# Kernel optimization log

Measured on AMD Instinct MI355X. Metric: run time of the kernel, lower is better.

## Reference

```python
import jax, jax.numpy as jnp
import numpy as np

B, L, H, V = 32, 2048, 128, 32000
ALPHA = 0.95
GATE_THRESH = 0.7
LN_EPS = 1e-5
NORM_EPS = 1e-12


def setup_inputs() -> dict:
    key = jax.random.key(0)
    ks = jax.random.split(key, 12)
    s = 0.02
    return {
        "seq": jax.random.randint(ks[0], (B, L), 0, V),
        "embed_w": jax.random.normal(ks[1], (V, H), jnp.float32) * s,
        "ff_w1": jax.random.normal(ks[2], (2 * H, H), jnp.float32) * s,
        "ff_b1": jnp.zeros((2 * H,), jnp.float32),
        "ff_w2": jax.random.normal(ks[3], (H, 2 * H), jnp.float32) * s,
        "ff_b2": jnp.zeros((H,), jnp.float32),
        "ln_g": jnp.ones((H,), jnp.float32),
        "ln_b": jnp.zeros((H,), jnp.float32),
        "kp_w": jax.random.normal(ks[4], (H, H), jnp.float32) * s,
        "rp_w": jax.random.normal(ks[5], (H, H), jnp.float32) * s,
        "rp_b": jnp.zeros((H,), jnp.float32),
        "out_w": jax.random.normal(ks[6], (V, H), jnp.float32) * s,
        "out_b": jnp.zeros((V,), jnp.float32),
    }


def reference(seq, embed_w, ff_w1, ff_b1, ff_w2, ff_b2, ln_g, ln_b,
              kp_w, rp_w, rp_b, out_w, out_b):
    h = embed_w[seq]                                    # (B,L,H)
    ff = jnp.maximum(h @ ff_w1.T + ff_b1, 0.0) @ ff_w2.T + ff_b2
    x = h + ff
    mu = jnp.mean(x, axis=-1, keepdims=True)
    var = jnp.mean((x - mu) ** 2, axis=-1, keepdims=True)
    h = (x - mu) * jax.lax.rsqrt(var + LN_EPS) * ln_g + ln_b

    k_all = jnp.einsum('blh,oh->blo', h, kp_w)          # kp(h), (B,L,H)
    ks_seq = jnp.transpose(k_all[:, :-1, :], (1, 0, 2)) # (L-1,B,H)

    def step(M, k):
        kn = k / jnp.maximum(jnp.linalg.norm(k, axis=-1, keepdims=True), NORM_EPS)
        vp = jnp.einsum('bij,bj->bi', M, kn)
        err = k - vp
        fire = (jnp.linalg.norm(err, axis=-1)
                >= GATE_THRESH * jnp.linalg.norm(k, axis=-1)).astype(k.dtype)
        delta = fire[:, None, None] * err[:, :, None] * kn[:, None, :]
        return M + (1.0 - ALPHA) * delta, None

    M0 = jnp.zeros((B, H, H), h.dtype)
    M, _ = jax.lax.scan(step, M0, ks_seq)

    q = k_all[:, -1, :]                                 # (B,H)
    read = jnp.einsum('bij,bj->bi', M, q)
    r = read @ rp_w.T + rp_b
    return r @ out_w.T + out_b                          # (B,V)
```

## Files before the change

kernel.cpp:

```cpp
#include <hip/hip_runtime.h>
#include <hip/hip_fp16.h>

#define B_  32
#define L_  2048
#define H_  128
#define H2_ 256
#define V_  32000
#define NT_ (B_*L_)
#define TOKS_PER_BLK 64
#define W_  32
#define NW_ (L_/W_)

template<int CTRL, int RMASK>
__device__ __forceinline__ float dpp_add(float x) {
    int v = __builtin_amdgcn_update_dpp(0, __float_as_int(x), CTRL, RMASK, 0xf, true);
    return x + __int_as_float(v);
}
__device__ __forceinline__ float wave_sum63(float x) {
    x = dpp_add<0x111, 0xf>(x);
    x = dpp_add<0x112, 0xf>(x);
    x = dpp_add<0x114, 0xf>(x);
    x = dpp_add<0x118, 0xf>(x);
    x = dpp_add<0x142, 0xa>(x);
    x = dpp_add<0x143, 0xc>(x);
    return x;
}
__device__ __forceinline__ float wave_allsum(float x) {
    x = wave_sum63(x);
    return __int_as_float(__builtin_amdgcn_readlane(__float_as_int(x), 63));
}
__device__ __forceinline__ float quad_sum(float x) {
    int v = __builtin_amdgcn_update_dpp(0, __float_as_int(x), 0xB1, 0xf, 0xf, true);
    x += __int_as_float(v);
    v = __builtin_amdgcn_update_dpp(0, __float_as_int(x), 0x4E, 0xf, 0xf, true);
    return x + __int_as_float(v);
}
__device__ __forceinline__ float sum16_hi(float x) {
    x = dpp_add<0x111, 0xf>(x);
    x = dpp_add<0x112, 0xf>(x);
    x = dpp_add<0x114, 0xf>(x);
    x = dpp_add<0x118, 0xf>(x);
    return x;
}

__global__ __launch_bounds__(256, 2) void ka_ff_ln_kp(
    const int*   __restrict__ seq,   const float* __restrict__ embed_w,
    const float* __restrict__ ff_w1, const float* __restrict__ ff_b1,
    const float* __restrict__ ff_w2, const float* __restrict__ ff_b2,
    const float* __restrict__ ln_g,  const float* __restrict__ ln_b,
    const float* __restrict__ kp_w,  float* __restrict__ k_all)
{
    __shared__ __half2 w1p[64][256];
    __shared__ float2 h2[128];
    __shared__ float2 y12[256];
    __shared__ float  p_sh[2][2][128];
    __shared__ float2 hln2[128];
    __shared__ float  red_sh[8];

    const int tid  = threadIdx.x;
    const int half = tid >> 7;
    const int i    = tid & 127;
    const int lane = tid & 63;
    const int wave = tid >> 6;

    for (int idx = tid; idx < 64*256; idx += 256) {
        int o = idx >> 6, j2 = idx & 63;
        float2 ab = *(const float2*)(ff_w1 + o*128 + 2*j2);
        w1p[j2][o] = __floats2half2_rn(ab.x, ab.y);
    }
    __half2 w2r[64];
    {
        const float* src = ff_w2 + (size_t)i*H2_ + half*128;
        #pragma unroll
        for (int q4 = 0; q4 < 16; ++q4) {
            float4 a = *(const float4*)(src + q4*8);
            float4 b = *(const float4*)(src + q4*8 + 4);
            w2r[q4*4+0] = __floats2half2_rn(a.x, a.y);
            w2r[q4*4+1] = __floats2half2_rn(a.z, a.w);
            w2r[q4*4+2] = __floats2half2_rn(b.x, b.y);
            w2r[q4*4+3] = __floats2half2_rn(b.z, b.w);
        }
    }
    float kreg[64];
    {
        const float* src = kp_w + (size_t)i*H_ + half*64;
        #pragma unroll
        for (int j4 = 0; j4 < 16; ++j4) {
            float4 v = *(const float4*)(src + j4*4);
            kreg[j4*4+0]=v.x; kreg[j4*4+1]=v.y; kreg[j4*4+2]=v.z; kreg[j4*4+3]=v.w;
        }
    }
    const float b1v = ff_b1[tid];
    const float b2v = ff_b2[i];
    const float gv  = ln_g[i];
    const float bv  = ln_b[i];
    __syncthreads();

    const int base = blockIdx.x * TOKS_PER_BLK;
    for (int it = 0; it < TOKS_PER_BLK; it += 2) {
        const int t0 = base + it;
        if (tid < 64) {
            int tok = tid >> 5;
            int l32 = tid & 31;
            int v   = seq[t0 + tok];
            float4 hv = *(const float4*)(embed_w + (size_t)v*H_ + l32*4);
            ((float*)&h2[l32*4+0])[tok] = hv.x;
            ((float*)&h2[l32*4+1])[tok] = hv.y;
            ((float*)&h2[l32*4+2])[tok] = hv.z;
            ((float*)&h2[l32*4+3])[tok] = hv.w;
        }
        __syncthreads();
        float a0 = b1v, a1 = b1v;
        #pragma unroll
        for (int j2 = 0; j2 < 64; ++j2) {
            __half2 w = w1p[j2][tid];
            float4 hh = *(const float4*)&h2[2*j2];
            float wl = __low2float(w), wh = __high2float(w);
            a0 = fmaf(wl, hh.x, a0); a0 = fmaf(wh, hh.z, a0);
            a1 = fmaf(wl, hh.y, a1); a1 = fmaf(wh, hh.w, a1);
        }
        y12[tid] = make_float2(fmaxf(a0, 0.f), fmaxf(a1, 0.f));
        __syncthreads();
        float c0 = 0.f, c1 = 0.f;
        #pragma unroll
        for (int q = 0; q < 64; ++q) {
            __half2 w = w2r[q];
            float4 yy = *(const float4*)&y12[half*128 + 2*q];
            float wl = __low2float(w), wh = __high2float(w);
            c0 = fmaf(wl, yy.x, c0); c0 = fmaf(wh, yy.z, c0);
            c1 = fmaf(wl, yy.y, c1); c1 = fmaf(wh, yy.w, c1);
        }
        p_sh[half][0][i] = c0;
        p_sh[half][1][i] = c1;
        __syncthreads();
        float x = ((const float*)&h2[i])[half] + p_sh[0][half][i] + p_sh[1][half][i] + b2v;
        {
            float s = x, s2 = x*x;
            #pragma unroll
            for (int m = 1; m <= 32; m <<= 1) {
                s  += __shfl_xor(s,  m);
                s2 += __shfl_xor(s2, m);
            }
            if (lane == 0) { red_sh[wave*2] = s; red_sh[wave*2+1] = s2; }
        }
        __syncthreads();
        float mu  = (red_sh[half*4+0] + red_sh[half*4+2]) * (1.0f/128.0f);
        float ex2 = (red_sh[half*4+1] + red_sh[half*4+3]) * (1.0f/128.0f);
        float var = ex2 - mu*mu;
        float rstd = 1.0f / sqrtf(var + 1e-5f);
        float hln = (x - mu) * rstd * gv + bv;
        ((float*)&hln2[i])[half] = hln;
        __syncthreads();
        float k0 = 0.f, k1 = 0.f;
        #pragma unroll
        for (int jj = 0; jj < 64; ++jj) {
            float2 hh = hln2[half*64 + jj];
            k0 = fmaf(kreg[jj], hh.x, k0);
            k1 = fmaf(kreg[jj], hh.y, k1);
        }
        p_sh[half][0][i] = k0;
        p_sh[half][1][i] = k1;
        __syncthreads();
        if (tid < 128) {
            k_all[(size_t)t0*H_     + i] = p_sh[0][0][i] + p_sh[1][0][i];
            k_all[(size_t)(t0+1)*H_ + i] = p_sh[0][1][i] + p_sh[1][1][i];
        }
    }
}

__global__ __launch_bounds__(512, 2) void kc_scan(
    const float* __restrict__ k_all, const float* __restrict__ rp_w,
    const float* __restrict__ rp_b,  float* __restrict__ r_out)
{
    __shared__ __align__(16) float kch[2][W_*H_];
    __shared__ __align__(16) float P_lds[W_][H_];
    __shared__ __align__(16) float G_T[W_][34];
    __shared__ __align__(16) float escT[H_][34];
    __shared__ __align__(16) float read_sh[H_];
    __shared__ float pr_sh[2][H_];

    const int b    = blockIdx.x;
    const int tid  = threadIdx.x;
    const int lane = tid & 63;
    const int wv   = tid >> 6;
    const int r    = tid >> 2;
    const int s    = tid & 3;
    const int cb   = s << 5;
    const int gi   = tid >> 4;
    const int gc   = (tid & 15) << 3;

    const float* kb = k_all + (size_t)b * (L_*H_);

    float Mreg[32];
    #pragma unroll
    for (int m = 0; m < 32; ++m) Mreg[m] = 0.f;

    {
        float4 a = *(const float4*)(kb + tid*8);
        float4 c = *(const float4*)(kb + tid*8 + 4);
        *(float4*)&kch[0][tid*8]     = a;
        *(float4*)&kch[0][tid*8 + 4] = c;
    }
    __syncthreads();

    #pragma unroll 1
    for (int w = 0; w < NW_; ++w) {
        const int buf = w & 1;
        const float* kcur = kch[buf];
        const float* kprv = kch[buf^1];

        float4 st0, st1;
        if (w + 1 < NW_) {
            const float* src = kb + (size_t)(w+1)*(W_*H_) + tid*8;
            st0 = *(const float4*)(src);
            st1 = *(const float4*)(src + 4);
        }

        if (w > 0) {
            #pragma unroll
            for (int j2 = 0; j2 < 16; ++j2) {
                float2 e2 = *(const float2*)&escT[r][2*j2];
                const float* ka0 = kprv + (2*j2)*H_ + cb;
                const float* ka1 = kprv + (2*j2+1)*H_ + cb;
                #pragma unroll
                for (int m8 = 0; m8 < 8; ++m8) {
                    const int a = ((m8 + 2*s) & 7) << 2;
                    float4 kv0 = *(const float4*)(ka0 + a);
                    float4 kv1 = *(const float4*)(ka1 + a);
                    Mreg[m8*4+0] = fmaf(e2.x, kv0.x, Mreg[m8*4+0]);
                    Mreg[m8*4+1] = fmaf(e2.x, kv0.y, Mreg[m8*4+1]);
                    Mreg[m8*4+2] = fmaf(e2.x, kv0.z, Mreg[m8*4+2]);
                    Mreg[m8*4+3] = fmaf(e2.x, kv0.w, Mreg[m8*4+3]);
                    Mreg[m8*4+0] = fmaf(e2.y, kv1.x, Mreg[m8*4+0]);
                    Mreg[m8*4+1] = fmaf(e2.y, kv1.y, Mreg[m8*4+1]);
                    Mreg[m8*4+2] = fmaf(e2.y, kv1.z, Mreg[m8*4+2]);
                    Mreg[m8*4+3] = fmaf(e2.y, kv1.w, Mreg[m8*4+3]);
                }
            }
        }
        __syncthreads();

        if (w + 1 < NW_) {
            *(float4*)&kch[buf^1][tid*8]     = st0;
            *(float4*)&kch[buf^1][tid*8 + 4] = st1;
        }

        {
            float4 kia = *(const float4*)(kcur + gi*H_ + gc);
            float4 kib = *(const float4*)(kcur + gi*H_ + gc + 4);
            #pragma unroll
            for (int j = 0; j < W_; ++j) {
                const float* kj = kcur + j*H_;
                float p0=0.f, p1=0.f, p2=0.f, p3=0.f;
                #pragma unroll
                for (int m8 = 0; m8 < 8; ++m8) {
                    const int a = ((m8 + 2*s) & 7) << 2;
                    float4 kv = *(const float4*)(kj + cb + a);
                    p0 = fmaf(Mreg[m8*4+0], kv.x, p0);
                    p1 = fmaf(Mreg[m8*4+1], kv.y, p1);
                    p2 = fmaf(Mreg[m8*4+2], kv.z, p2);
                    p3 = fmaf(Mreg[m8*4+3], kv.w, p3);
                }
                float p = quad_sum((p0+p1) + (p2+p3));
                if (s == 0) P_lds[j][r] = p;
                float4 ga = *(const float4*)(kj + gc);
                float4 gb = *(const float4*)(kj + gc + 4);
                float g0 = kia.x*ga.x + kia.y*ga.y;
                g0 = fmaf(kia.z, ga.z, g0); g0 = fmaf(kia.w, ga.w, g0);
                float g1 = kib.x*gb.x + kib.y*gb.y;
                g1 = fmaf(kib.z, gb.z, g1); g1 = fmaf(kib.w, gb.w, g1);
                float g = sum16_hi(g0 + g1);
                if ((tid & 15) == 15) G_T[j][gi] = g;
            }
        }
        __syncthreads();

        if (wv == 0) {
            const int last = (w == NW_-1);
            #pragma unroll
            for (int j = 0; j < W_; ++j) {
                float nk2 = G_T[j][j];
                float rn  = 1.0f / fmaxf(sqrtf(nk2), 1e-12f);
                float t0 = P_lds[j][lane];
                float t1 = P_lds[j][lane + 64];
                float k0 = kcur[j*H_ + lane];
                float k1 = kcur[j*H_ + 64 + lane];
                #pragma unroll
                for (int i2 = 0; i2 < ((j+1)>>1); ++i2) {
                    float2 g2 = *(const float2*)&G_T[j][2*i2];
                    float2 ea = *(const float2*)&escT[lane][2*i2];
                    float2 eb = *(const float2*)&escT[lane+64][2*i2];
                    t0 = fmaf(g2.x, ea.x, t0); t1 = fmaf(g2.x, eb.x, t1);
                    if (2*i2+1 < j) {
                        t0 = fmaf(g2.y, ea.y, t0); t1 = fmaf(g2.y, eb.y, t1);
                    }
                }
                if (last && j == W_-1) {
                    read_sh[lane]      = t0;
                    read_sh[lane + 64] = t1;
                } else {
                    float e0 = fmaf(-rn, t0, k0);
                    float e1 = fmaf(-rn, t1, k1);
                    float es = wave_allsum(fmaf(e0, e0, e1*e1));
                    float sc = (es >= 0.49f * nk2) ? 0.05f * rn : 0.f;
                    escT[lane][j]      = sc * e0;
                    escT[lane + 64][j] = sc * e1;
                }
            }
        }
        __syncthreads();
    }

    if (tid < 256) {
        const int o  = tid & 127;
        const int hf = tid >> 7;
        float acc = 0.f;
        #pragma unroll
        for (int j4 = 0; j4 < 16; ++j4) {
            float4 wvv = *(const float4*)(rp_w + (size_t)o*H_ + hf*64 + j4*4);
            float4 rv  = *(const float4*)&read_sh[hf*64 + j4*4];
            acc = fmaf(wvv.x, rv.x, acc);
            acc = fmaf(wvv.y, rv.y, acc);
            acc = fmaf(wvv.z, rv.z, acc);
            acc = fmaf(wvv.w, rv.w, acc);
        }
        pr_sh[hf][o] = acc;
    }
    __syncthreads();
    if (tid < 128) r_out[b*H_ + tid] = pr_sh[0][tid] + pr_sh[1][tid] + rp_b[tid];
}

__global__ __launch_bounds__(256) void kd_out(
    const float* __restrict__ r_in, const float* __restrict__ out_w,
    const float* __restrict__ out_b, float* __restrict__ out)
{
    __shared__ float r_sh[B_ * H_];
    const int tid = threadIdx.x;
    for (int idx = tid; idx < B_*H_; idx += 256) r_sh[idx] = r_in[idx];
    __syncthreads();
    const int v = blockIdx.x * 256 + tid;
    const float* wrow = out_w + (size_t)v * H_;
    float acc[B_];
    #pragma unroll
    for (int bb = 0; bb < B_; ++bb) acc[bb] = 0.f;
    for (int h4 = 0; h4 < H_/4; ++h4) {
        float4 w = *(const float4*)(wrow + h4*4);
        #pragma unroll
        for (int bb = 0; bb < B_; ++bb) {
            const float* rr = &r_sh[bb*H_ + h4*4];
            acc[bb] = fmaf(w.x, rr[0], acc[bb]);
            acc[bb] = fmaf(w.y, rr[1], acc[bb]);
            acc[bb] = fmaf(w.z, rr[2], acc[bb]);
            acc[bb] = fmaf(w.w, rr[3], acc[bb]);
        }
    }
    const float bias = out_b[v];
    #pragma unroll
    for (int bb = 0; bb < B_; ++bb) out[(size_t)bb*V_ + v] = acc[bb] + bias;
}

extern "C" void kernel_launch(void* const* d_in, const int* in_sizes, int n_in,
                              void* d_out, int out_size, void* d_ws, size_t ws_size,
                              hipStream_t stream)
{
    const int*   seq     = (const int*)  d_in[0];
    const float* embed_w = (const float*)d_in[1];
    const float* ff_w1   = (const float*)d_in[2];
    const float* ff_b1   = (const float*)d_in[3];
    const float* ff_w2   = (const float*)d_in[4];
    const float* ff_b2   = (const float*)d_in[5];
    const float* ln_g    = (const float*)d_in[6];
    const float* ln_b    = (const float*)d_in[7];
    const float* kp_w    = (const float*)d_in[8];
    const float* rp_w    = (const float*)d_in[9];
    const float* rp_b    = (const float*)d_in[10];
    const float* out_w   = (const float*)d_in[11];
    const float* out_b   = (const float*)d_in[12];
    float* out = (float*)d_out;

    float* k_all = (float*)d_ws;
    float* r_buf = k_all + (size_t)NT_ * H_;

    ka_ff_ln_kp<<<dim3(NT_/TOKS_PER_BLK), dim3(256), 0, stream>>>(
        seq, embed_w, ff_w1, ff_b1, ff_w2, ff_b2, ln_g, ln_b, kp_w, k_all);
    kc_scan<<<dim3(B_), dim3(512), 0, stream>>>(k_all, rp_w, rp_b, r_buf);
    kd_out<<<dim3(V_/256), dim3(256), 0, stream>>>(r_buf, out_w, out_b, out);
}
```

Before: 1.932 ms.

## Restructure scan kernel to 1024 threads with overlapped Gram computation

The scan kernel now runs with 1024 threads, and each thread holds a 2x8 tile of M instead of a 32-wide row slice. This removes the quad reduction in favour of 16-lane reductions. The Gram matrix for the next window is computed by waves 1-8 while wave 0 runs the serial error recurrence, so it leaves the critical path. Wave 0 keeps the error vectors in registers and reads Gram entries through readlane rather than LDS. The k chunks use padded rows to avoid LDS bank conflicts. In exchange the kernel raises register pressure in wave 0 and adds work at its wider launch.

Result: faster. 1.637 ms (-15.3%).

```diff
diff --git a/kernel.cpp b/kernel.cpp
--- a/kernel.cpp
+++ b/kernel.cpp
@@ -10,6 +10,7 @@
 #define TOKS_PER_BLK 64
 #define W_  32
 #define NW_ (L_/W_)
+#define KROW 132
 
 template<int CTRL, int RMASK>
 __device__ __forceinline__ float dpp_add(float x) {
@@ -28,12 +29,6 @@
 __device__ __forceinline__ float wave_allsum(float x) {
     x = wave_sum63(x);
     return __int_as_float(__builtin_amdgcn_readlane(__float_as_int(x), 63));
-}
-__device__ __forceinline__ float quad_sum(float x) {
-    int v = __builtin_amdgcn_update_dpp(0, __float_as_int(x), 0xB1, 0xf, 0xf, true);
-    x += __int_as_float(v);
-    v = __builtin_amdgcn_update_dpp(0, __float_as_int(x), 0x4E, 0xf, 0xf, true);
-    return x + __int_as_float(v);
 }
 __device__ __forceinline__ float sum16_hi(float x) {
     x = dpp_add<0x111, 0xf>(x);
@@ -168,145 +163,169 @@
     }
 }
 
-__global__ __launch_bounds__(512, 2) void kc_scan(
+__global__ __launch_bounds__(1024, 4) void kc_scan(
     const float* __restrict__ k_all, const float* __restrict__ rp_w,
     const float* __restrict__ rp_b,  float* __restrict__ r_out)
 {
-    __shared__ __align__(16) float kch[2][W_*H_];
+    __shared__ __align__(16) float kch[2][W_*KROW];
     __shared__ __align__(16) float P_lds[W_][H_];
-    __shared__ __align__(16) float G_T[W_][34];
-    __shared__ __align__(16) float escT[H_][34];
+    __shared__ __align__(16) float escT[W_][H_];
+    __shared__ __align__(16) float G_lds[2][64][16];
     __shared__ __align__(16) float read_sh[H_];
     __shared__ float pr_sh[2][H_];
 
-    const int b    = blockIdx.x;
     const int tid  = threadIdx.x;
     const int lane = tid & 63;
     const int wv   = tid >> 6;
-    const int r    = tid >> 2;
-    const int s    = tid & 3;
-    const int cb   = s << 5;
-    const int gi   = tid >> 4;
-    const int gc   = (tid & 15) << 3;
-
-    const float* kb = k_all + (size_t)b * (L_*H_);
-
-    float Mreg[32];
+    const int ct   = tid & 15;
+    const int rt   = tid >> 4;
+    const int cb   = ct << 3;
+    const int srow = tid >> 5;
+    const int scol = (tid & 31) << 2;
+
+    const float* kb = k_all + (size_t)blockIdx.x * (L_*H_);
+
+    float M0[8], M1[8];
     #pragma unroll
-    for (int m = 0; m < 32; ++m) Mreg[m] = 0.f;
+    for (int c = 0; c < 8; ++c) { M0[c] = 0.f; M1[c] = 0.f; }
 
     {
-        float4 a = *(const float4*)(kb + tid*8);
-        float4 c = *(const float4*)(kb + tid*8 + 4);
-        *(float4*)&kch[0][tid*8]     = a;
-        *(float4*)&kch[0][tid*8 + 4] = c;
+        float4 v = *(const float4*)(kb + tid*4);
+        *(float4*)&kch[0][srow*KROW + scol] = v;
+    }
+    __syncthreads();
+
+    if (wv >= 1 && wv <= 8) {
+        const int p0i = (wv-1)*128 + lane*2;
+        const int gi  = p0i >> 5;
+        const int gj0 = p0i & 31;
+        const float* ki  = &kch[0][gi*KROW];
+        const float* kj0 = &kch[0][gj0*KROW];
+        const float* kj1 = &kch[0][(gj0+1)*KROW];
+        float d00=0,d01=0,d02=0,d03=0, d10=0,d11=0,d12=0,d13=0;
+        #pragma unroll 8
+        for (int c4 = 0; c4 < 32; ++c4) {
+            float4 x = *(const float4*)(ki  + c4*4);
+            float4 y = *(const float4*)(kj0 + c4*4);
+            float4 z = *(const float4*)(kj1 + c4*4);
+            d00=fmaf(x.x,y.x,d00); d01=fmaf(x.y,y.y,d01);
+            d02=fmaf(x.z,y.z,d02); d03=fmaf(x.w,y.w,d03);
+            d10=fmaf(x.x,z.x,d10); d11=fmaf(x.y,z.y,d11);
+            d12=fmaf(x.z,z.z,d12); d13=fmaf(x.w,z.w,d13);
+        }
+        G_lds[0][gi     ][gj0>>1] = (d00+d01)+(d02+d03);
+        G_lds[0][gi + 32][gj0>>1] = (d10+d11)+(d12+d13);
     }
     __syncthreads();
 
     #pragma unroll 1
     for (int w = 0; w < NW_; ++w) {
         const int buf = w & 1;
-        const float* kcur = kch[buf];
-        const float* kprv = kch[buf^1];
-
-        float4 st0, st1;
-        if (w + 1 < NW_) {
-            const float* src = kb + (size_t)(w+1)*(W_*H_) + tid*8;
-            st0 = *(const float4*)(src);
-            st1 = *(const float4*)(src + 4);
-        }
+        const float* kcur = &kch[buf][0];
+        const float* kprv = &kch[buf^1][0];
+        const bool hn = (w + 1 < NW_);
+        float4 stg;
+        if (hn) stg = *(const float4*)(kb + (size_t)(w+1)*(W_*H_) + tid*4);
 
         if (w > 0) {
+            #pragma unroll 8
+            for (int j = 0; j < W_; ++j) {
+                float2 e2 = *(const float2*)&escT[j][2*rt];
+                const float* kr = kprv + j*KROW + cb;
+                float4 a  = *(const float4*)(kr);
+                float4 b2 = *(const float4*)(kr + 4);
+                M0[0]=fmaf(e2.x,a.x,M0[0]);  M0[1]=fmaf(e2.x,a.y,M0[1]);
+                M0[2]=fmaf(e2.x,a.z,M0[2]);  M0[3]=fmaf(e2.x,a.w,M0[3]);
+                M0[4]=fmaf(e2.x,b2.x,M0[4]); M0[5]=fmaf(e2.x,b2.y,M0[5]);
+                M0[6]=fmaf(e2.x,b2.z,M0[6]); M0[7]=fmaf(e2.x,b2.w,M0[7]);
+                M1[0]=fmaf(e2.y,a.x,M1[0]);  M1[1]=fmaf(e2.y,a.y,M1[1]);
+                M1[2]=fmaf(e2.y,a.z,M1[2]);  M1[3]=fmaf(e2.y,a.w,M1[3]);
+                M1[4]=fmaf(e2.y,b2.x,M1[4]); M1[5]=fmaf(e2.y,b2.y,M1[5]);
+                M1[6]=fmaf(e2.y,b2.z,M1[6]); M1[7]=fmaf(e2.y,b2.w,M1[7]);
+            }
+        }
+        __syncthreads();
+        if (hn) *(float4*)&kch[buf^1][srow*KROW + scol] = stg;
+
+        #pragma unroll 8
+        for (int j = 0; j < W_; ++j) {
+            const float* kr = kcur + j*KROW + cb;
+            float4 a  = *(const float4*)(kr);
+            float4 b2 = *(const float4*)(kr + 4);
+            float p0 = M0[0]*a.x;
+            p0=fmaf(M0[1],a.y,p0);  p0=fmaf(M0[2],a.z,p0);  p0=fmaf(M0[3],a.w,p0);
+            p0=fmaf(M0[4],b2.x,p0); p0=fmaf(M0[5],b2.y,p0);
+            p0=fmaf(M0[6],b2.z,p0); p0=fmaf(M0[7],b2.w,p0);
+            float p1 = M1[0]*a.x;
+            p1=fmaf(M1[1],a.y,p1);  p1=fmaf(M1[2],a.z,p1);  p1=fmaf(M1[3],a.w,p1);
+            p1=fmaf(M1[4],b2.x,p1); p1=fmaf(M1[5],b2.y,p1);
+            p1=fmaf(M1[6],b2.z,p1); p1=fmaf(M1[7],b2.w,p1);
+            p0 = sum16_hi(p0);
+            p1 = sum16_hi(p1);
+            if (ct == 15) *(float2*)&P_lds[j][2*rt] = make_float2(p0, p1);
+        }
+        __syncthreads();
+
+        if (wv == 0) {
+            float Grf[16];
             #pragma unroll
-            for (int j2 = 0; j2 < 16; ++j2) {
-                float2 e2 = *(const float2*)&escT[r][2*j2];
-                const float* ka0 = kprv + (2*j2)*H_ + cb;
-                const float* ka1 = kprv + (2*j2+1)*H_ + cb;
-                #pragma unroll
-                for (int m8 = 0; m8 < 8; ++m8) {
-                    const int a = ((m8 + 2*s) & 7) << 2;
-                    float4 kv0 = *(const float4*)(ka0 + a);
-                    float4 kv1 = *(const float4*)(ka1 + a);
-                    Mreg[m8*4+0] = fmaf(e2.x, kv0.x, Mreg[m8*4+0]);
-                    Mreg[m8*4+1] = fmaf(e2.x, kv0.y, Mreg[m8*4+1]);
-                    Mreg[m8*4+2] = fmaf(e2.x, kv0.z, Mreg[m8*4+2]);
-                    Mreg[m8*4+3] = fmaf(e2.x, kv0.w, Mreg[m8*4+3]);
-                    Mreg[m8*4+0] = fmaf(e2.y, kv1.x, Mreg[m8*4+0]);
-                    Mreg[m8*4+1] = fmaf(e2.y, kv1.y, Mreg[m8*4+1]);
-                    Mreg[m8*4+2] = fmaf(e2.y, kv1.z, Mreg[m8*4+2]);
-                    Mreg[m8*4+3] = fmaf(e2.y, kv1.w, Mreg[m8*4+3]);
-                }
+            for (int p = 0; p < 4; ++p) {
+                float4 g4 = *(const float4*)&G_lds[buf][lane][4*p];
+                Grf[4*p+0]=g4.x; Grf[4*p+1]=g4.y; Grf[4*p+2]=g4.z; Grf[4*p+3]=g4.w;
             }
-        }
-        __syncthreads();
-
-        if (w + 1 < NW_) {
-            *(float4*)&kch[buf^1][tid*8]     = st0;
-            *(float4*)&kch[buf^1][tid*8 + 4] = st1;
-        }
-
-        {
-            float4 kia = *(const float4*)(kcur + gi*H_ + gc);
-            float4 kib = *(const float4*)(kcur + gi*H_ + gc + 4);
+            float e0[W_], e1[W_];
+            const bool lastw = (w == NW_-1);
             #pragma unroll
             for (int j = 0; j < W_; ++j) {
-                const float* kj = kcur + j*H_;
-                float p0=0.f, p1=0.f, p2=0.f, p3=0.f;
-                #pragma unroll
-                for (int m8 = 0; m8 < 8; ++m8) {
-                    const int a = ((m8 + 2*s) & 7) << 2;
-                    float4 kv = *(const float4*)(kj + cb + a);
-                    p0 = fmaf(Mreg[m8*4+0], kv.x, p0);
-                    p1 = fmaf(Mreg[m8*4+1], kv.y, p1);
-                    p2 = fmaf(Mreg[m8*4+2], kv.z, p2);
-                    p3 = fmaf(Mreg[m8*4+3], kv.w, p3);
-                }
-                float p = quad_sum((p0+p1) + (p2+p3));
-                if (s == 0) P_lds[j][r] = p;
-                float4 ga = *(const float4*)(kj + gc);
-                float4 gb = *(const float4*)(kj + gc + 4);
-                float g0 = kia.x*ga.x + kia.y*ga.y;
-                g0 = fmaf(kia.z, ga.z, g0); g0 = fmaf(kia.w, ga.w, g0);
-                float g1 = kib.x*gb.x + kib.y*gb.y;
-                g1 = fmaf(kib.z, gb.z, g1); g1 = fmaf(kib.w, gb.w, g1);
-                float g = sum16_hi(g0 + g1);
-                if ((tid & 15) == 15) G_T[j][gi] = g;
-            }
-        }
-        __syncthreads();
-
-        if (wv == 0) {
-            const int last = (w == NW_-1);
-            #pragma unroll
-            for (int j = 0; j < W_; ++j) {
-                float nk2 = G_T[j][j];
-                float rn  = 1.0f / fmaxf(sqrtf(nk2), 1e-12f);
                 float t0 = P_lds[j][lane];
                 float t1 = P_lds[j][lane + 64];
-                float k0 = kcur[j*H_ + lane];
-                float k1 = kcur[j*H_ + 64 + lane];
                 #pragma unroll
-                for (int i2 = 0; i2 < ((j+1)>>1); ++i2) {
-                    float2 g2 = *(const float2*)&G_T[j][2*i2];
-                    float2 ea = *(const float2*)&escT[lane][2*i2];
-                    float2 eb = *(const float2*)&escT[lane+64][2*i2];
-                    t0 = fmaf(g2.x, ea.x, t0); t1 = fmaf(g2.x, eb.x, t1);
-                    if (2*i2+1 < j) {
-                        t0 = fmaf(g2.y, ea.y, t0); t1 = fmaf(g2.y, eb.y, t1);
-                    }
+                for (int i = 0; i < j; ++i) {
+                    float g = __int_as_float(__builtin_amdgcn_readlane(
+                        __float_as_int(Grf[j>>1]), i + ((j&1)<<5)));
+                    t0 = fmaf(g, e0[i], t0);
+                    t1 = fmaf(g, e1[i], t1);
                 }
-                if (last && j == W_-1) {
+                float nk2 = __int_as_float(__builtin_amdgcn_readlane(
+                        __float_as_int(Grf[j>>1]), j + ((j&1)<<5)));
+                if (lastw && j == W_-1) {
                     read_sh[lane]      = t0;
                     read_sh[lane + 64] = t1;
                 } else {
-                    float e0 = fmaf(-rn, t0, k0);
-                    float e1 = fmaf(-rn, t1, k1);
-                    float es = wave_allsum(fmaf(e0, e0, e1*e1));
-                    float sc = (es >= 0.49f * nk2) ? 0.05f * rn : 0.f;
-                    escT[lane][j]      = sc * e0;
-                    escT[lane + 64][j] = sc * e1;
+                    float rn  = 1.0f / fmaxf(sqrtf(nk2), 1e-12f);
+                    float k0  = kcur[j*KROW + lane];
+                    float k1  = kcur[j*KROW + 64 + lane];
+                    float ev0 = fmaf(-rn, t0, k0);
+                    float ev1 = fmaf(-rn, t1, k1);
+                    float es  = wave_allsum(fmaf(ev0, ev0, ev1*ev1));
+                    float sc  = (es >= 0.49f * nk2) ? 0.05f * rn : 0.f;
+                    e0[j] = sc * ev0;
+                    e1[j] = sc * ev1;
+                    escT[j][lane]      = e0[j];
+                    escT[j][lane + 64] = e1[j];
                 }
             }
+        } else if (wv <= 8 && hn) {
+            const float* kt = &kch[buf^1][0];
+            const int p0i = (wv-1)*128 + lane*2;
+            const int gi  = p0i >> 5;
+            const int gj0 = p0i & 31;
+            const float* ki  = kt + gi*KROW;
+            const float* kj0 = kt + gj0*KROW;
+            const float* kj1 = kt + (gj0+1)*KROW;
+            float d00=0,d01=0,d02=0,d03=0, d10=0,d11=0,d12=0,d13=0;
+            #pragma unroll 8
+            for (int c4 = 0; c4 < 32; ++c4) {
+                float4 x = *(const float4*)(ki  + c4*4);
+                float4 y = *(const float4*)(kj0 + c4*4);
+                float4 z = *(const float4*)(kj1 + c4*4);
+                d00=fmaf(x.x,y.x,d00); d01=fmaf(x.y,y.y,d01);
+                d02=fmaf(x.z,y.z,d02); d03=fmaf(x.w,y.w,d03);
+                d10=fmaf(x.x,z.x,d10); d11=fmaf(x.y,z.y,d11);
+                d12=fmaf(x.z,z.z,d12); d13=fmaf(x.w,z.w,d13);
+            }
+            G_lds[buf^1][gi     ][gj0>>1] = (d00+d01)+(d02+d03);
+            G_lds[buf^1][gi + 32][gj0>>1] = (d10+d11)+(d12+d13);
         }
         __syncthreads();
     }
@@ -327,7 +346,7 @@
         pr_sh[hf][o] = acc;
     }
     __syncthreads();
-    if (tid < 128) r_out[b*H_ + tid] = pr_sh[0][tid] + pr_sh[1][tid] + rp_b[tid];
+    if (tid < 128) r_out[blockIdx.x*H_ + tid] = pr_sh[0][tid] + pr_sh[1][tid] + rp_b[tid];
 }
 
 __global__ __launch_bounds__(256) void kd_out(
@@ -383,6 +402,6 @@
 
     ka_ff_ln_kp<<<dim3(NT_/TOKS_PER_BLK), dim3(256), 0, stream>>>(
         seq, embed_w, ff_w1, ff_b1, ff_w2, ff_b2, ln_g, ln_b, kp_w, k_all);
-    kc_scan<<<dim3(B_), dim3(512), 0, stream>>>(k_all, rp_w, rp_b, r_buf);
+    kc_scan<<<dim3(B_), dim3(1024), 0, stream>>>(k_all, rp_w, rp_b, r_buf);
     kd_out<<<dim3(V_/256), dim3(256), 0, stream>>>(r_buf, out_w, out_b, out);
 }
```
